# Kernel optimization log

Measured on AMD Instinct MI355X. Metric: run time of the kernel, lower is better.

The kernel has to match this reference:

```python
import jax, jax.numpy as jnp
import numpy as np

B, N, D, H, DG = 1, 1024, 512, 8, 64
DK = D // H
EPS = 1e-5


def _layer_norm(x, g, b):
    m = jnp.mean(x, axis=-1, keepdims=True)
    v = jnp.var(x, axis=-1, keepdims=True)
    return (x - m) / jnp.sqrt(v + EPS) * g + b


def _box_rel_embedding(box):
    # box: (B, N, 4) = x_min, y_min, x_max, y_max
    x_min, y_min, x_max, y_max = [box[..., i] for i in range(4)]  # each (B, N)
    cx = (x_min + x_max) * 0.5
    cy = (y_min + y_max) * 0.5
    w = x_max - x_min + 1.0
    h = y_max - y_min + 1.0
    dx = jnp.log(jnp.clip(jnp.abs((cx[:, :, None] - cx[:, None, :]) / w[:, :, None]), 0.001))
    dy = jnp.log(jnp.clip(jnp.abs((cy[:, :, None] - cy[:, None, :]) / h[:, :, None]), 0.001))
    dw = jnp.log(w[:, :, None] / w[:, None, :])
    dh = jnp.log(h[:, :, None] / h[:, None, :])
    pos = jnp.stack([dx, dy, dw, dh], axis=-1)  # (B, N, N, 4)
    dim_mat = 1.0 / jnp.power(1000.0, jnp.arange(DG // 8, dtype=jnp.float32) / (DG // 8))  # (8,)
    mul = (100.0 * pos[..., None] * dim_mat).reshape(pos.shape[0], pos.shape[1], pos.shape[2], -1)  # (B,N,N,32)
    return jnp.concatenate([jnp.sin(mul), jnp.cos(mul)], axis=-1)  # (B, N, N, 64)


def _split_heads(x, W, b):
    # torch permute(2,0,1,3).view(-1, len, d_k): head-major flattening
    return (x @ W.T + b).reshape(B, N, H, DK).transpose(2, 0, 1, 3).reshape(H * B, N, DK)


def _forward(input_query, input_key, input_value, input_box,
             Wq, bq, Wk, bk, Wv, bv, Wo, bo, WG_w, WG_b,
             ln0_g, ln0_b, ln_g, ln_b):
    residual = input_query
    emb = _box_rel_embedding(input_box)  # (B, N, N, 64)
    # per-head linear (64 -> 1) then relu: (B, H, N, N)
    w_g = jax.nn.relu(jnp.einsum('bijg,hg->bhij', emb, WG_w) + WG_b[None, :, None, None])
    q = _split_heads(input_query, Wq, bq)  # (H*B, N, DK)
    k = _split_heads(input_key, Wk, bk)
    v = _split_heads(input_value, Wv, bv)
    scores = jnp.einsum('xnd,xmd->xnm', q, k) / np.sqrt(DK).astype(np.float32)  # (H*B, N, N)
    # original adds (B,H,N,N) to (H*B,N,N): only valid for B==1
    w_mn = jax.nn.softmax(jnp.log(jnp.clip(w_g.reshape(H * B, N, N), 1e-6)) + scores, axis=-1)
    x = jnp.einsum('xnm,xmd->xnd', w_mn, v)  # (H*B, N, DK)
    # faithful to original: transpose(1,2) then view(nbatches, -1, h*d_k)
    x = x.transpose(0, 2, 1).reshape(B, -1, H * DK)  # (B, N, D)
    out0 = _layer_norm(x + residual, ln0_g, ln0_b)
    out = out0 @ Wo.T + bo  # dropout = identity (eval mode)
    return _layer_norm(out + out0, ln_g, ln_b)


def setup_inputs() -> dict:
    key = jax.random.key(0)
    ks = jax.random.split(key, 12)
    inp = {}
    inp['input_query'] = jax.random.normal(ks[0], (B, N, D), dtype=jnp.float32)
    inp['input_key'] = jax.random.normal(ks[1], (B, N, D), dtype=jnp.float32)
    inp['input_value'] = jax.random.normal(ks[2], (B, N, D), dtype=jnp.float32)
    mins = jax.random.uniform(ks[3], (B, N, 2), dtype=jnp.float32) * 500.0
    sizes = jax.random.uniform(ks[4], (B, N, 2), dtype=jnp.float32) * 99.0 + 1.0
    inp['input_box'] = jnp.concatenate([mins, mins + sizes], axis=-1)  # valid boxes
    s = 0.02
    inp['Wq'] = jax.random.normal(ks[5], (D, D), dtype=jnp.float32) * s
    inp['bq'] = jnp.zeros((D,), dtype=jnp.float32)
    inp['Wk'] = jax.random.normal(ks[6], (D, D), dtype=jnp.float32) * s
    inp['bk'] = jnp.zeros((D,), dtype=jnp.float32)
    inp['Wv'] = jax.random.normal(ks[7], (D, D), dtype=jnp.float32) * s
    inp['bv'] = jnp.zeros((D,), dtype=jnp.float32)
    inp['Wo'] = jax.random.normal(ks[8], (D, D), dtype=jnp.float32) * s
    inp['bo'] = jnp.zeros((D,), dtype=jnp.float32)
    inp['WG_w'] = jax.random.normal(ks[9], (H, DG), dtype=jnp.float32) * 0.1
    inp['WG_b'] = jax.random.normal(ks[10], (H,), dtype=jnp.float32) * 0.1
    inp['ln0_g'] = jnp.ones((D,), dtype=jnp.float32)
    inp['ln0_b'] = jnp.zeros((D,), dtype=jnp.float32)
    inp['ln_g'] = jnp.ones((D,), dtype=jnp.float32)
    inp['ln_b'] = jnp.zeros((D,), dtype=jnp.float32)
    return inp


def reference(input_query, input_key, input_value, input_box,
              Wq, bq, Wk, bk, Wv, bv, Wo, bo, WG_w, WG_b,
              ln0_g, ln0_b, ln_g, ln_b):
    return _forward(input_query, input_key, input_value, input_box,
                    Wq, bq, Wk, bk, Wv, bv, Wo, bo, WG_w, WG_b,
                    ln0_g, ln0_b, ln_g, ln_b)
```

## Files before the change

### kernel.cpp

```cpp
#include <hip/hip_runtime.h>
#include <cstddef>

#define NTOK 1024
#define DMODEL 512
#define NHEAD 8
#define DKH 64
#define NSPLIT 4
#define JQ 256

typedef __attribute__((ext_vector_type(4))) float f32x4;
typedef __attribute__((ext_vector_type(8))) __bf16 bf16x8;
typedef __attribute__((ext_vector_type(4))) __bf16 bf16x4;
typedef __attribute__((ext_vector_type(4))) unsigned short u16x4;
typedef __attribute__((ext_vector_type(8))) unsigned short u16x8;
typedef __attribute__((ext_vector_type(4))) _Float16 f16x4;
typedef unsigned short ushort_t;

__device__ __forceinline__ float wave_sum_f(float v){
  #pragma unroll
  for (int m=1; m<64; m<<=1) v += __shfl_xor(v, m, 64);
  return v;
}
__device__ __forceinline__ unsigned short f2bf(float f){
  __bf16 b = (__bf16)f;
  return __builtin_bit_cast(unsigned short, b);
}
__device__ __forceinline__ float bf2f(unsigned short u){
  return (float)__builtin_bit_cast(__bf16, u);
}

__device__ __forceinline__ float fract_hw(float x){
  float r; asm("v_fract_f32 %0, %1" : "=v"(r) : "v"(x)); return r;
}
__device__ __forceinline__ float sin_rev(float rev){
  float f = fract_hw(rev);
  float s; asm("v_sin_f32 %0, %1" : "=v"(s) : "v"(f)); return s;
}
__device__ __forceinline__ float cos_rev(float rev){
  float f = fract_hw(rev);
  float c; asm("v_cos_f32 %0, %1" : "=v"(c) : "v"(f)); return c;
}
__device__ __forceinline__ float log_hw(float x){
  float l; asm("v_log_f32 %0, %1" : "=v"(l) : "v"(x));
  return 0.69314718056f * l;
}
__device__ __forceinline__ float exp_hw(float x){
  float y = x * 1.44269504f;
  float e; asm("v_exp_f32 %0, %1" : "=v"(e) : "v"(y));
  return e;
}

__global__ __launch_bounds__(256) void k_front2(
    const float* __restrict__ box, const float* __restrict__ WGw, const float* __restrict__ WGb,
    _Float16* __restrict__ wg16,
    const float* __restrict__ inq, const float* __restrict__ ink, const float* __restrict__ inv,
    const float* __restrict__ Wq, const float* __restrict__ Wk, const float* __restrict__ Wv,
    const float* __restrict__ Wo,
    const float* __restrict__ bq, const float* __restrict__ bk, const float* __restrict__ bv,
    ushort_t* __restrict__ Qb, ushort_t* __restrict__ Kb, ushort_t* __restrict__ Vt,
    ushort_t* __restrict__ Wob){
  __shared__ __align__(16) char smem[17408];
  const int t = threadIdx.x;
  const int lane = t & 63, w = t >> 6, li = lane & 15, g = lane >> 4;
  if (blockIdx.x >= 1408){
    int off = ((blockIdx.x - 1408)*256 + t)*8;
    float4 a = *(const float4*)(Wo + off);
    float4 b4 = *(const float4*)(Wo + off + 4);
    u16x4 o0, o1;
    o0[0]=f2bf(a.x); o0[1]=f2bf(a.y); o0[2]=f2bf(a.z); o0[3]=f2bf(a.w);
    o1[0]=f2bf(b4.x); o1[1]=f2bf(b4.y); o1[2]=f2bf(b4.z); o1[3]=f2bf(b4.w);
    *(u16x4*)(Wob + off) = o0;
    *(u16x4*)(Wob + off + 4) = o1;
    return;
  }
  if (blockIdx.x >= 1024){
    const int u = blockIdx.x - 1024;
    const int z = u >> 7;
    const int rem = u & 127;
    const int m0 = (rem >> 3)*64;
    const int n0 = (rem & 7)*64;
    const float* A = z==0 ? inq : z==1 ? ink : inv;
    const float* W = z==0 ? Wq : z==1 ? Wk : Wv;
    const float* bias = z==0 ? bq : z==1 ? bk : bv;
    ushort_t* Al = (ushort_t*)smem;
    ushort_t* Wl = (ushort_t*)(smem + 8704);
    const int row = t >> 2, kq = (t & 3)*16;
    const int mrb = (w >> 1)*32;
    const int nrb = (w & 1)*32;
    f32x4 acc[2][2] = {};
    for (int k0 = 0; k0 < DMODEL; k0 += 64){
      {
        const float* ap = A + (size_t)(m0+row)*DMODEL + k0 + kq;
        const float* wp = W + (size_t)(n0+row)*DMODEL + k0 + kq;
        #pragma unroll
        for (int q=0; q<4; q++){
          float4 av = *(const float4*)(ap + q*4);
          float4 wv = *(const float4*)(wp + q*4);
          u16x4 pa, pw;
          pa[0]=f2bf(av.x); pa[1]=f2bf(av.y); pa[2]=f2bf(av.z); pa[3]=f2bf(av.w);
          pw[0]=f2bf(wv.x); pw[1]=f2bf(wv.y); pw[2]=f2bf(wv.z); pw[3]=f2bf(wv.w);
          *(u16x4*)(Al + row*68 + kq + q*4) = pa;
          *(u16x4*)(Wl + row*68 + kq + q*4) = pw;
        }
      }
      __syncthreads();
      #pragma unroll
      for (int kc=0; kc<64; kc+=32){
        const ushort_t* arl = Al + (mrb + li)*68 + kc + g*8;
        const ushort_t* wrl = Wl + (nrb + li)*68 + kc + g*8;
        bf16x8 af0 = *(const bf16x8*)(arl);
        bf16x8 af1 = *(const bf16x8*)(arl + 16*68);
        bf16x8 wf0 = *(const bf16x8*)(wrl);
        bf16x8 wf1 = *(const bf16x8*)(wrl + 16*68);
        if (z < 2){
          acc[0][0] = __builtin_amdgcn_mfma_f32_16x16x32_bf16(wf0, af0, acc[0][0], 0,0,0);
          acc[0][1] = __builtin_amdgcn_mfma_f32_16x16x32_bf16(wf0, af1, acc[0][1], 0,0,0);
          acc[1][0] = __builtin_amdgcn_mfma_f32_16x16x32_bf16(wf1, af0, acc[1][0], 0,0,0);
          acc[1][1] = __builtin_amdgcn_mfma_f32_16x16x32_bf16(wf1, af1, acc[1][1], 0,0,0);
        } else {
          acc[0][0] = __builtin_amdgcn_mfma_f32_16x16x32_bf16(af0, wf0, acc[0][0], 0,0,0);
          acc[0][1] = __builtin_amdgcn_mfma_f32_16x16x32_bf16(af0, wf1, acc[0][1], 0,0,0);
          acc[1][0] = __builtin_amdgcn_mfma_f32_16x16x32_bf16(af1, wf0, acc[1][0], 0,0,0);
          acc[1][1] = __builtin_amdgcn_mfma_f32_16x16x32_bf16(af1, wf1, acc[1][1], 0,0,0);
        }
      }
      __syncthreads();
    }
    if (z < 2){
      ushort_t* C = z ? Kb : Qb;
      #pragma unroll
      for (int nf=0; nf<2; nf++){
        int n = n0 + nrb + nf*16 + g*4;
        float4 b4 = *(const float4*)(bias + n);
        const float* bp = (const float*)&b4;
        #pragma unroll
        for (int mf=0; mf<2; mf++){
          int m = m0 + mrb + mf*16 + li;
          u16x4 o;
          #pragma unroll
          for (int r=0; r<4; r++) o[r] = f2bf(acc[nf][mf][r] + bp[r]);
          *(u16x4*)(C + (size_t)m*DMODEL + n) = o;
        }
      }
    } else {
      #pragma unroll
      for (int mf=0; mf<2; mf++){
        int m = m0 + mrb + mf*16 + g*4;
        #pragma unroll
        for (int nf=0; nf<2; nf++){
          int n = n0 + nrb + nf*16 + li;
          float bn = bias[n];
          u16x4 o;
          #pragma unroll
          for (int r=0; r<4; r++) o[r] = f2bf(acc[mf][nf][r] + bn);
          *(u16x4*)(Vt + (((size_t)(n>>6))<<16) + ((size_t)(n&63)<<10) + m) = o;
        }
      }
    }
    return;
  }
  float* arr = (float*)smem;
  #pragma unroll
  for (int u2=0; u2<4; u2++){
    int idx = u2*256 + t;
    float4 b4 = *(const float4*)(box + idx*4);
    arr[idx]        = (b4.x + b4.z)*0.5f;
    arr[1024+idx]   = (b4.y + b4.w)*0.5f;
    arr[2048+idx]   = log_hw(b4.z - b4.x + 1.0f);
    arr[3072+idx]   = log_hw(b4.w - b4.y + 1.0f);
  }
  const int i = blockIdx.x;
  float4 bi = *(const float4*)(box + i*4);
  float wi = bi.z - bi.x + 1.0f, hi = bi.w - bi.y + 1.0f;
  float Pi = (g==0) ? (bi.x+bi.z)*0.5f : (g==1) ? (bi.y+bi.w)*0.5f
           : (g==2) ? log_hw(wi) : log_hw(hi);
  float Ri = (g==0) ? 1.0f/wi : (g==1) ? 1.0f/hi : 1.0f;
  const bool doLog = (g < 2);
  bf16x8 wfs = {}, wfc = {};
  float wgb_li = 0.0f;
  if (li < 8){
    #pragma unroll
    for (int e=0; e<8; e++){
      wfs[e] = (__bf16)WGw[li*64 + g*8 + e];
      wfc[e] = (__bf16)WGw[li*64 + 32 + g*8 + e];
    }
    wgb_li = WGb[li];
  }
  __syncthreads();
  const float* parr = arr + g*1024;
  const float DMrev[8] = {15.9154943f, 6.7115094f, 2.8302196f, 1.1934938f,
                          0.5032921f, 0.2122365f, 0.08949941f, 0.0377416f};
  const int jbeg = w*256;
  for (int it=0; it<16; ++it){
    int j = jbeg + it*16 + li;
    float diff = (Pi - parr[j])*Ri;
    float lg = log_hw(fmaxf(fabsf(diff), 1e-3f));
    float dv = doLog ? lg : diff;
    bf16x8 afs, afc;
    #pragma unroll
    for (int e=0; e<8; e++){
      float rev = dv * DMrev[e];
      afs[e] = (__bf16)sin_rev(rev);
      afc[e] = (__bf16)cos_rev(rev);
    }
    f32x4 acc = (f32x4){0.f,0.f,0.f,0.f};
    acc = __builtin_amdgcn_mfma_f32_16x16x32_bf16(afs, wfs, acc, 0,0,0);
    acc = __builtin_amdgcn_mfma_f32_16x16x32_bf16(afc, wfc, acc, 0,0,0);
    if (li < 8){
      f16x4 o;
      #pragma unroll
      for (int r=0; r<4; r++)
        o[r] = (_Float16)fmaxf(acc[r] + wgb_li, 6.103515625e-05f);
      *(f16x4*)(wg16 + (((size_t)li<<20) + ((size_t)i<<10) + jbeg + it*16 + g*4)) = o;
    }
  }
}

__global__ __launch_bounds__(512) void k_attn3(const ushort_t* __restrict__ Qb,
     const ushort_t* __restrict__ Kb, const ushort_t* __restrict__ Vt,
     const _Float16* __restrict__ wg, ushort_t* __restrict__ Xpt, float* __restrict__ rsp){
  __shared__ ushort_t Ks[256*68];
  __shared__ ushort_t Vs[64*264];
  const int t = threadIdx.x;
  const int itg = blockIdx.x, h = blockIdx.y, sp = blockIdx.z;
  const int jbeg = sp*JQ;
  {
    const int r = t >> 3, c = (t & 7)*8;
    #pragma unroll
    for (int p=0; p<4; p++){
      u16x8 kv = *(const u16x8*)(Kb + (size_t)(jbeg + p*64 + r)*DMODEL + h*DKH + c);
      *(u16x8*)(Ks + (p*64 + r)*68 + c) = kv;
      u16x8 vv = *(const u16x8*)(Vt + ((size_t)h<<16) + (size_t)r*NTOK + jbeg + p*64 + c);
      *(u16x8*)(Vs + r*264 + p*64 + c) = vv;
    }
  }
  const int lane = t & 63, w = t >> 6;
  const int i0 = (itg*8 + w)*16;
  const int li = lane & 15, g = lane >> 4;
  const ushort_t* qp = Qb + (size_t)(i0+li)*DMODEL + h*DKH + g*8;
  bf16x8 qf0 = *(const bf16x8*)(qp);
  bf16x8 qf1 = *(const bf16x8*)(qp + 32);
  const _Float16* gbase = wg + ((size_t)h<<20) + ((size_t)(i0+li)<<10) + jbeg + g*4;
  f32x4 xacc[4];
  #pragma unroll
  for (int mf=0; mf<4; mf++) xacc[mf] = (f32x4){0.f,0.f,0.f,0.f};
  float rsum = 0.f;
  __syncthreads();
  #pragma unroll
  for (int jj = 0; jj < JQ; jj += 32){
    const ushort_t* kp = Ks + (jj + li)*68 + g*8;
    bf16x8 a00 = *(const bf16x8*)(kp);
    bf16x8 a01 = *(const bf16x8*)(kp + 32);
    bf16x8 a10 = *(const bf16x8*)(kp + 16*68);
    bf16x8 a11 = *(const bf16x8*)(kp + 16*68 + 32);
    f32x4 s0 = (f32x4){0.f,0.f,0.f,0.f};
    f32x4 s1 = (f32x4){0.f,0.f,0.f,0.f};
    s0 = __builtin_amdgcn_mfma_f32_16x16x32_bf16(a00, qf0, s0, 0,0,0);
    s0 = __builtin_amdgcn_mfma_f32_16x16x32_bf16(a01, qf1, s0, 0,0,0);
    s1 = __builtin_amdgcn_mfma_f32_16x16x32_bf16(a10, qf0, s1, 0,0,0);
    s1 = __builtin_amdgcn_mfma_f32_16x16x32_bf16(a11, qf1, s1, 0,0,0);
    f16x4 g0 = *(const f16x4*)(gbase + jj);
    f16x4 g1 = *(const f16x4*)(gbase + jj + 16);
    float p[8];
    #pragma unroll
    for (int r=0; r<4; r++){ p[r]   = (float)g0[r] * exp_hw(s0[r]*0.125f); rsum += p[r]; }
    #pragma unroll
    for (int r=0; r<4; r++){ p[4+r] = (float)g1[r] * exp_hw(s1[r]*0.125f); rsum += p[4+r]; }
    bf16x8 pb;
    pb[0]=(__bf16)p[0]; pb[1]=(__bf16)p[1]; pb[2]=(__bf16)p[2]; pb[3]=(__bf16)p[3];
    pb[4]=(__bf16)p[4]; pb[5]=(__bf16)p[5]; pb[6]=(__bf16)p[6]; pb[7]=(__bf16)p[7];
    #pragma unroll
    for (int mf=0; mf<4; mf++){
      const ushort_t* vp = Vs + (size_t)(li + mf*16)*264 + jj + g*4;
      bf16x4 lo = *(const bf16x4*)(vp);
      bf16x4 hi = *(const bf16x4*)(vp + 16);
      bf16x8 vf = __builtin_shufflevector(lo, hi, 0,1,2,3,4,5,6,7);
      xacc[mf] = __builtin_amdgcn_mfma_f32_16x16x32_bf16(vf, pb, xacc[mf], 0,0,0);
    }
  }
  rsum += __shfl_xor(rsum, 16, 64);
  rsum += __shfl_xor(rsum, 32, 64);
  if (lane < 16) rsp[((size_t)sp*NHEAD + h)*NTOK + i0 + li] = rsum;
  __syncthreads();
  float* xw = (float*)Ks + w*(16*68);
  #pragma unroll
  for (int mf=0; mf<4; mf++)
    *(f32x4*)&xw[li*68 + mf*16 + g*4] = xacc[mf];
  __builtin_amdgcn_s_waitcnt(0);
  float xv[16];
  #pragma unroll
  for (int r=0; r<16; r++) xv[r] = xw[r*68 + lane];
  u16x8 o0, o1;
  #pragma unroll
  for (int r=0; r<8; r++){ o0[r] = f2bf(xv[r]); o1[r] = f2bf(xv[8+r]); }
  ushort_t* xp = Xpt + (((size_t)sp*NHEAD + h)*DKH + lane)*NTOK + i0;
  *(u16x8*)(xp)     = o0;
  *(u16x8*)(xp + 8) = o1;
}

__global__ __launch_bounds__(512) void k_back2(
    const ushort_t* __restrict__ Xpt, const float* __restrict__ rsp,
    const float* __restrict__ inq,
    const float* __restrict__ ln0g, const float* __restrict__ ln0b,
    const ushort_t* __restrict__ Wob, const float* __restrict__ bo,
    const float* __restrict__ lng, const float* __restrict__ lnb,
    float* __restrict__ out){
  __shared__ ushort_t Ab[8][520];
  __shared__ float    Y[8][516];
  __shared__ float    red[8][8][2];
  const int t = threadIdx.x, lane = t & 63, w = t >> 6;
  const int li = lane & 15, g = lane >> 4;
  const int m0 = blockIdx.x*8;
  {
    const int n = m0 + w;
    const int h = n >> 7, dk = (n >> 1) & 63, mo = (n & 1)*512;
    float x[8];
    float sum = 0.f, sq = 0.f;
    #pragma unroll
    for (int c=0; c<8; c++){
      int d = c*64 + lane;
      int i = mo + d;
      float sv = 0.f, rv = 0.f;
      #pragma unroll
      for (int sp=0; sp<NSPLIT; sp++){
        sv += bf2f(Xpt[(((size_t)sp*NHEAD + h)*DKH + dk)*NTOK + i]);
        rv += rsp[((size_t)sp*NHEAD + h)*NTOK + i];
      }
      x[c] = sv/rv + inq[(size_t)n*DMODEL + d];
      sum += x[c]; sq += x[c]*x[c];
    }
    sum = wave_sum_f(sum);
    sq  = wave_sum_f(sq);
    float mean = sum * (1.0f/512.0f);
    float var = sq * (1.0f/512.0f) - mean*mean;
    float rs = rsqrtf(var + 1e-5f);
    #pragma unroll
    for (int c=0; c<8; c++){
      int d = c*64 + lane;
      float y = (x[c]-mean)*rs*ln0g[d] + ln0b[d];
      Y[w][d] = y;
      Ab[w][d] = f2bf(y);
    }
  }
  __syncthreads();
  const int n0 = w*64;
  const ushort_t* ar = &Ab[li & 7][g*8];
  const ushort_t* wr = Wob + (size_t)(n0+li)*DMODEL + g*8;
  f32x4 acc[4] = {};
  #pragma unroll
  for (int k0=0; k0<DMODEL; k0+=64){
    bf16x8 afa = *(const bf16x8*)(ar + k0);
    bf16x8 afb = *(const bf16x8*)(ar + k0 + 32);
    #pragma unroll
    for (int nf=0; nf<4; nf++){
      const ushort_t* wp = wr + (size_t)nf*16*DMODEL + k0;
      bf16x8 wfa = *(const bf16x8*)(wp);
      bf16x8 wfb = *(const bf16x8*)(wp + 32);
      acc[nf] = __builtin_amdgcn_mfma_f32_16x16x32_bf16(wfa, afa, acc[nf], 0,0,0);
      acc[nf] = __builtin_amdgcn_mfma_f32_16x16x32_bf16(wfb, afb, acc[nf], 0,0,0);
    }
  }
  float s = 0.f, qq = 0.f;
  f32x4 v[4];
  #pragma unroll
  for (int nf=0; nf<4; nf++){
    int n = n0 + nf*16 + g*4;
    f32x4 b4 = *(const f32x4*)(bo + n);
    #pragma unroll
    for (int r=0; r<4; r++){
      float x = acc[nf][r] + b4[r] + Y[li & 7][n + r];
      v[nf][r] = x; s += x; qq += x*x;
    }
  }
  s  += __shfl_xor(s, 16, 64);  s  += __shfl_xor(s, 32, 64);
  qq += __shfl_xor(qq, 16, 64); qq += __shfl_xor(qq, 32, 64);
  if (g == 0 && li < 8){ red[w][li][0] = s; red[w][li][1] = qq; }
  __syncthreads();
  float S = 0.f, Q = 0.f;
  #pragma unroll
  for (int u=0; u<8; u++){ S += red[u][li & 7][0]; Q += red[u][li & 7][1]; }
  float mean = S * (1.0f/512.0f);
  float var = Q * (1.0f/512.0f) - mean*mean;
  float rs = rsqrtf(var + 1e-5f);
  if (li < 8){
    const int m = m0 + li;
    #pragma unroll
    for (int nf=0; nf<4; nf++){
      int n = n0 + nf*16 + g*4;
      f32x4 g4 = *(const f32x4*)(lng + n);
      f32x4 be = *(const f32x4*)(lnb + n);
      f32x4 o;
      #pragma unroll
      for (int r=0; r<4; r++) o[r] = (v[nf][r]-mean)*rs*g4[r] + be[r];
      *(f32x4*)(out + (size_t)m*DMODEL + n) = o;
    }
  }
}

extern "C" void kernel_launch(void* const* d_in, const int* in_sizes, int n_in,
                              void* d_out, int out_size, void* d_ws, size_t ws_size,
                              hipStream_t stream){
  (void)in_sizes; (void)n_in; (void)out_size; (void)ws_size;
  const float* in_q = (const float*)d_in[0];
  const float* in_k = (const float*)d_in[1];
  const float* in_v = (const float*)d_in[2];
  const float* box  = (const float*)d_in[3];
  const float* Wq   = (const float*)d_in[4];
  const float* bq   = (const float*)d_in[5];
  const float* Wk   = (const float*)d_in[6];
  const float* bk   = (const float*)d_in[7];
  const float* Wv   = (const float*)d_in[8];
  const float* bv   = (const float*)d_in[9];
  const float* Wo   = (const float*)d_in[10];
  const float* bo   = (const float*)d_in[11];
  const float* WGw  = (const float*)d_in[12];
  const float* WGb  = (const float*)d_in[13];
  const float* ln0g = (const float*)d_in[14];
  const float* ln0b = (const float*)d_in[15];
  const float* lng  = (const float*)d_in[16];
  const float* lnb  = (const float*)d_in[17];

  float* ws = (float*)d_ws;
  ushort_t* Wob  = (ushort_t*)(ws + 0);
  ushort_t* Qb   = (ushort_t*)(ws + 131072);
  ushort_t* Kb   = (ushort_t*)(ws + 393216);
  ushort_t* Vt   = (ushort_t*)(ws + 655360);
  _Float16* wg16 = (_Float16*)(ws + 917504);
  ushort_t* Xpt  = (ushort_t*)(ws + 5111808);
  float*    rsp  = ws + 6160384;
  float*    out  = (float*)d_out;

  k_front2<<<dim3(1536), dim3(256), 0, stream>>>(box, WGw, WGb, wg16,
            in_q, in_k, in_v, Wq, Wk, Wv, Wo, bq, bk, bv, Qb, Kb, Vt, Wob);
  k_attn3<<<dim3(8,8,4), dim3(512), 0, stream>>>(Qb, Kb, Vt, wg16, Xpt, rsp);
  k_back2<<<dim3(128), dim3(512), 0, stream>>>(Xpt, rsp, in_q, ln0g, ln0b,
            Wob, bo, lng, lnb, out);
}
```

Before: 66.73 us.

## Merge three kernels into one persistent launch with atomic counter barriers

Folds the front, attention and back kernels into a single 1664-block launch at 512 threads. Blocks signal completion through global atomic counters, and the attention and back-end blocks spin on those counters before they start. Front blocks are reshaped to 512 threads, with each QKV GEMM block doing two tiles. This aims to remove inter-kernel launch gaps and tail drain, but it adds a memset launch, spin-wait overhead, a large shared-memory footprint that limits occupancy, and a deadlock risk if waiting blocks are resident before their producers.

```diff
diff --git a/kernel.cpp b/kernel.cpp
--- a/kernel.cpp
+++ b/kernel.cpp
@@ -50,7 +50,20 @@
   return e;
 }
 
-__global__ __launch_bounds__(256) void k_front2(
+__device__ __forceinline__ void mark_done(unsigned* c){
+  __syncthreads();
+  if (threadIdx.x == 0)
+    __hip_atomic_fetch_add(c, 1u, __ATOMIC_RELEASE, __HIP_MEMORY_SCOPE_AGENT);
+}
+__device__ __forceinline__ void wait_for(unsigned* c, unsigned target){
+  if (threadIdx.x == 0){
+    while (__hip_atomic_load(c, __ATOMIC_ACQUIRE, __HIP_MEMORY_SCOPE_AGENT) < target)
+      __builtin_amdgcn_s_sleep(8);
+  }
+  __syncthreads();
+}
+
+__global__ __launch_bounds__(512) void k_all(
     const float* __restrict__ box, const float* __restrict__ WGw, const float* __restrict__ WGb,
     _Float16* __restrict__ wg16,
     const float* __restrict__ inq, const float* __restrict__ ink, const float* __restrict__ inv,
@@ -58,35 +71,91 @@
     const float* __restrict__ Wo,
     const float* __restrict__ bq, const float* __restrict__ bk, const float* __restrict__ bv,
     ushort_t* __restrict__ Qb, ushort_t* __restrict__ Kb, ushort_t* __restrict__ Vt,
-    ushort_t* __restrict__ Wob){
-  __shared__ __align__(16) char smem[17408];
+    ushort_t* __restrict__ Wob,
+    ushort_t* __restrict__ Xpt, float* __restrict__ rsp,
+    const float* __restrict__ ln0g, const float* __restrict__ ln0b,
+    const float* __restrict__ bo, const float* __restrict__ lng, const float* __restrict__ lnb,
+    float* __restrict__ out, unsigned* bar){
+  __shared__ __align__(16) char smem[68608];
   const int t = threadIdx.x;
+  const int b = blockIdx.x;
   const int lane = t & 63, w = t >> 6, li = lane & 15, g = lane >> 4;
-  if (blockIdx.x >= 1408){
-    int off = ((blockIdx.x - 1408)*256 + t)*8;
-    float4 a = *(const float4*)(Wo + off);
-    float4 b4 = *(const float4*)(Wo + off + 4);
-    u16x4 o0, o1;
-    o0[0]=f2bf(a.x); o0[1]=f2bf(a.y); o0[2]=f2bf(a.z); o0[3]=f2bf(a.w);
-    o1[0]=f2bf(b4.x); o1[1]=f2bf(b4.y); o1[2]=f2bf(b4.z); o1[3]=f2bf(b4.w);
-    *(u16x4*)(Wob + off) = o0;
-    *(u16x4*)(Wob + off + 4) = o1;
+
+  if (b < 1024){
+    float* arr = (float*)smem;
+    #pragma unroll
+    for (int u2=0; u2<2; u2++){
+      int idx = u2*512 + t;
+      float4 b4 = *(const float4*)(box + idx*4);
+      arr[idx]        = (b4.x + b4.z)*0.5f;
+      arr[1024+idx]   = (b4.y + b4.w)*0.5f;
+      arr[2048+idx]   = log_hw(b4.z - b4.x + 1.0f);
+      arr[3072+idx]   = log_hw(b4.w - b4.y + 1.0f);
+    }
+    const int i = b;
+    float4 bi = *(const float4*)(box + i*4);
+    float wi = bi.z - bi.x + 1.0f, hi = bi.w - bi.y + 1.0f;
+    float Pi = (g==0) ? (bi.x+bi.z)*0.5f : (g==1) ? (bi.y+bi.w)*0.5f
+             : (g==2) ? log_hw(wi) : log_hw(hi);
+    float Ri = (g==0) ? 1.0f/wi : (g==1) ? 1.0f/hi : 1.0f;
+    const bool doLog = (g < 2);
+    bf16x8 wfs = {}, wfc = {};
+    float wgb_li = 0.0f;
+    if (li < 8){
+      #pragma unroll
+      for (int e=0; e<8; e++){
+        wfs[e] = (__bf16)WGw[li*64 + g*8 + e];
+        wfc[e] = (__bf16)WGw[li*64 + 32 + g*8 + e];
+      }
+      wgb_li = WGb[li];
+    }
+    __syncthreads();
+    const float* parr = arr + g*1024;
+    const float DMrev[8] = {15.9154943f, 6.7115094f, 2.8302196f, 1.1934938f,
+                            0.5032921f, 0.2122365f, 0.08949941f, 0.0377416f};
+    const int jbeg = w*128;
+    for (int it=0; it<8; ++it){
+      int j = jbeg + it*16 + li;
+      float diff = (Pi - parr[j])*Ri;
+      float lg = log_hw(fmaxf(fabsf(diff), 1e-3f));
+      float dv = doLog ? lg : diff;
+      bf16x8 afs, afc;
+      #pragma unroll
+      for (int e=0; e<8; e++){
+        float rev = dv * DMrev[e];
+        afs[e] = (__bf16)sin_rev(rev);
+        afc[e] = (__bf16)cos_rev(rev);
+      }
+      f32x4 acc = (f32x4){0.f,0.f,0.f,0.f};
+      acc = __builtin_amdgcn_mfma_f32_16x16x32_bf16(afs, wfs, acc, 0,0,0);
+      acc = __builtin_amdgcn_mfma_f32_16x16x32_bf16(afc, wfc, acc, 0,0,0);
+      if (li < 8){
+        f16x4 o;
+        #pragma unroll
+        for (int r=0; r<4; r++)
+          o[r] = (_Float16)fmaxf(acc[r] + wgb_li, 6.103515625e-05f);
+        *(f16x4*)(wg16 + (((size_t)li<<20) + ((size_t)i<<10) + jbeg + it*16 + g*4)) = o;
+      }
+    }
+    mark_done(bar);
     return;
   }
-  if (blockIdx.x >= 1024){
-    const int u = blockIdx.x - 1024;
-    const int z = u >> 7;
-    const int rem = u & 127;
+  if (b < 1216){
+    const int unit = (b - 1024)*2 + (w >> 2);
+    const int z = unit >> 7;
+    const int rem = unit & 127;
     const int m0 = (rem >> 3)*64;
     const int n0 = (rem & 7)*64;
     const float* A = z==0 ? inq : z==1 ? ink : inv;
     const float* W = z==0 ? Wq : z==1 ? Wk : Wv;
     const float* bias = z==0 ? bq : z==1 ? bk : bv;
-    ushort_t* Al = (ushort_t*)smem;
-    ushort_t* Wl = (ushort_t*)(smem + 8704);
-    const int row = t >> 2, kq = (t & 3)*16;
-    const int mrb = (w >> 1)*32;
-    const int nrb = (w & 1)*32;
+    ushort_t* Al = (ushort_t*)(smem + (w>>2)*17408);
+    ushort_t* Wl = (ushort_t*)(smem + (w>>2)*17408 + 8704);
+    const int t2 = t & 255;
+    const int row = t2 >> 2, kq = (t2 & 3)*16;
+    const int w2 = w & 3;
+    const int mrb = (w2 >> 1)*32;
+    const int nrb = (w2 & 1)*32;
     f32x4 acc[2][2] = {};
     for (int k0 = 0; k0 < DMODEL; k0 += 64){
       {
@@ -157,242 +226,190 @@
         }
       }
     }
+    mark_done(bar);
     return;
   }
-  float* arr = (float*)smem;
-  #pragma unroll
-  for (int u2=0; u2<4; u2++){
-    int idx = u2*256 + t;
-    float4 b4 = *(const float4*)(box + idx*4);
-    arr[idx]        = (b4.x + b4.z)*0.5f;
-    arr[1024+idx]   = (b4.y + b4.w)*0.5f;
-    arr[2048+idx]   = log_hw(b4.z - b4.x + 1.0f);
-    arr[3072+idx]   = log_hw(b4.w - b4.y + 1.0f);
-  }
-  const int i = blockIdx.x;
-  float4 bi = *(const float4*)(box + i*4);
-  float wi = bi.z - bi.x + 1.0f, hi = bi.w - bi.y + 1.0f;
-  float Pi = (g==0) ? (bi.x+bi.z)*0.5f : (g==1) ? (bi.y+bi.w)*0.5f
-           : (g==2) ? log_hw(wi) : log_hw(hi);
-  float Ri = (g==0) ? 1.0f/wi : (g==1) ? 1.0f/hi : 1.0f;
-  const bool doLog = (g < 2);
-  bf16x8 wfs = {}, wfc = {};
-  float wgb_li = 0.0f;
-  if (li < 8){
-    #pragma unroll
-    for (int e=0; e<8; e++){
-      wfs[e] = (__bf16)WGw[li*64 + g*8 + e];
-      wfc[e] = (__bf16)WGw[li*64 + 32 + g*8 + e];
-    }
-    wgb_li = WGb[li];
-  }
-  __syncthreads();
-  const float* parr = arr + g*1024;
-  const float DMrev[8] = {15.9154943f, 6.7115094f, 2.8302196f, 1.1934938f,
-                          0.5032921f, 0.2122365f, 0.08949941f, 0.0377416f};
-  const int jbeg = w*256;
-  for (int it=0; it<16; ++it){
-    int j = jbeg + it*16 + li;
-    float diff = (Pi - parr[j])*Ri;
-    float lg = log_hw(fmaxf(fabsf(diff), 1e-3f));
-    float dv = doLog ? lg : diff;
-    bf16x8 afs, afc;
-    #pragma unroll
-    for (int e=0; e<8; e++){
-      float rev = dv * DMrev[e];
-      afs[e] = (__bf16)sin_rev(rev);
-      afc[e] = (__bf16)cos_rev(rev);
-    }
-    f32x4 acc = (f32x4){0.f,0.f,0.f,0.f};
-    acc = __builtin_amdgcn_mfma_f32_16x16x32_bf16(afs, wfs, acc, 0,0,0);
-    acc = __builtin_amdgcn_mfma_f32_16x16x32_bf16(afc, wfc, acc, 0,0,0);
-    if (li < 8){
-      f16x4 o;
-      #pragma unroll
-      for (int r=0; r<4; r++)
-        o[r] = (_Float16)fmaxf(acc[r] + wgb_li, 6.103515625e-05f);
-      *(f16x4*)(wg16 + (((size_t)li<<20) + ((size_t)i<<10) + jbeg + it*16 + g*4)) = o;
-    }
-  }
-}
-
-__global__ __launch_bounds__(512) void k_attn3(const ushort_t* __restrict__ Qb,
-     const ushort_t* __restrict__ Kb, const ushort_t* __restrict__ Vt,
-     const _Float16* __restrict__ wg, ushort_t* __restrict__ Xpt, float* __restrict__ rsp){
-  __shared__ ushort_t Ks[256*68];
-  __shared__ ushort_t Vs[64*264];
-  const int t = threadIdx.x;
-  const int itg = blockIdx.x, h = blockIdx.y, sp = blockIdx.z;
-  const int jbeg = sp*JQ;
+  if (b < 1280){
+    int off = ((b - 1216)*512 + t)*8;
+    float4 a = *(const float4*)(Wo + off);
+    float4 b4 = *(const float4*)(Wo + off + 4);
+    u16x4 o0, o1;
+    o0[0]=f2bf(a.x); o0[1]=f2bf(a.y); o0[2]=f2bf(a.z); o0[3]=f2bf(a.w);
+    o1[0]=f2bf(b4.x); o1[1]=f2bf(b4.y); o1[2]=f2bf(b4.z); o1[3]=f2bf(b4.w);
+    *(u16x4*)(Wob + off) = o0;
+    *(u16x4*)(Wob + off + 4) = o1;
+    mark_done(bar);
+    return;
+  }
+  if (b < 1536){
+    wait_for(bar, 1280u);
+    ushort_t* Ks = (ushort_t*)smem;
+    ushort_t* Vs = (ushort_t*)(smem + 34816);
+    const int bb = b - 1280;
+    const int itg = bb & 7, h = (bb >> 3) & 7, sp = bb >> 6;
+    const int jbeg = sp*JQ;
+    {
+      const int r = t >> 3, c = (t & 7)*8;
+      #pragma unroll
+      for (int p=0; p<4; p++){
+        u16x8 kv = *(const u16x8*)(Kb + (size_t)(jbeg + p*64 + r)*DMODEL + h*DKH + c);
+        *(u16x8*)(Ks + (p*64 + r)*68 + c) = kv;
+        u16x8 vv = *(const u16x8*)(Vt + ((size_t)h<<16) + (size_t)r*NTOK + jbeg + p*64 + c);
+        *(u16x8*)(Vs + r*264 + p*64 + c) = vv;
+      }
+    }
+    const int i0 = (itg*8 + w)*16;
+    const ushort_t* qp = Qb + (size_t)(i0+li)*DMODEL + h*DKH + g*8;
+    bf16x8 qf0 = *(const bf16x8*)(qp);
+    bf16x8 qf1 = *(const bf16x8*)(qp + 32);
+    const _Float16* gbase = wg16 + ((size_t)h<<20) + ((size_t)(i0+li)<<10) + jbeg + g*4;
+    f32x4 xacc[4];
+    #pragma unroll
+    for (int mf=0; mf<4; mf++) xacc[mf] = (f32x4){0.f,0.f,0.f,0.f};
+    float rsum = 0.f;
+    __syncthreads();
+    #pragma unroll
+    for (int jj = 0; jj < JQ; jj += 32){
+      const ushort_t* kp = Ks + (jj + li)*68 + g*8;
+      bf16x8 a00 = *(const bf16x8*)(kp);
+      bf16x8 a01 = *(const bf16x8*)(kp + 32);
+      bf16x8 a10 = *(const bf16x8*)(kp + 16*68);
+      bf16x8 a11 = *(const bf16x8*)(kp + 16*68 + 32);
+      f32x4 s0 = (f32x4){0.f,0.f,0.f,0.f};
+      f32x4 s1 = (f32x4){0.f,0.f,0.f,0.f};
+      s0 = __builtin_amdgcn_mfma_f32_16x16x32_bf16(a00, qf0, s0, 0,0,0);
+      s0 = __builtin_amdgcn_mfma_f32_16x16x32_bf16(a01, qf1, s0, 0,0,0);
+      s1 = __builtin_amdgcn_mfma_f32_16x16x32_bf16(a10, qf0, s1, 0,0,0);
+      s1 = __builtin_amdgcn_mfma_f32_16x16x32_bf16(a11, qf1, s1, 0,0,0);
+      f16x4 g0 = *(const f16x4*)(gbase + jj);
+      f16x4 g1 = *(const f16x4*)(gbase + jj + 16);
+      float p[8];
+      #pragma unroll
+      for (int r=0; r<4; r++){ p[r]   = (float)g0[r] * exp_hw(s0[r]*0.125f); rsum += p[r]; }
+      #pragma unroll
+      for (int r=0; r<4; r++){ p[4+r] = (float)g1[r] * exp_hw(s1[r]*0.125f); rsum += p[4+r]; }
+      bf16x8 pb;
+      pb[0]=(__bf16)p[0]; pb[1]=(__bf16)p[1]; pb[2]=(__bf16)p[2]; pb[3]=(__bf16)p[3];
+      pb[4]=(__bf16)p[4]; pb[5]=(__bf16)p[5]; pb[6]=(__bf16)p[6]; pb[7]=(__bf16)p[7];
+      #pragma unroll
+      for (int mf=0; mf<4; mf++){
+        const ushort_t* vp = Vs + (size_t)(li + mf*16)*264 + jj + g*4;
+        bf16x4 lo = *(const bf16x4*)(vp);
+        bf16x4 hi = *(const bf16x4*)(vp + 16);
+        bf16x8 vf = __builtin_shufflevector(lo, hi, 0,1,2,3,4,5,6,7);
+        xacc[mf] = __builtin_amdgcn_mfma_f32_16x16x32_bf16(vf, pb, xacc[mf], 0,0,0);
+      }
+    }
+    rsum += __shfl_xor(rsum, 16, 64);
+    rsum += __shfl_xor(rsum, 32, 64);
+    if (lane < 16) rsp[((size_t)sp*NHEAD + h)*NTOK + i0 + li] = rsum;
+    __syncthreads();
+    float* xw = (float*)Ks + w*(16*68);
+    #pragma unroll
+    for (int mf=0; mf<4; mf++)
+      *(f32x4*)&xw[li*68 + mf*16 + g*4] = xacc[mf];
+    __builtin_amdgcn_s_waitcnt(0);
+    float xv[16];
+    #pragma unroll
+    for (int r=0; r<16; r++) xv[r] = xw[r*68 + lane];
+    u16x8 o0, o1;
+    #pragma unroll
+    for (int r=0; r<8; r++){ o0[r] = f2bf(xv[r]); o1[r] = f2bf(xv[8+r]); }
+    ushort_t* xp = Xpt + (((size_t)sp*NHEAD + h)*DKH + lane)*NTOK + i0;
+    *(u16x8*)(xp)     = o0;
+    *(u16x8*)(xp + 8) = o1;
+    mark_done(bar + 1);
+    return;
+  }
   {
-    const int r = t >> 3, c = (t & 7)*8;
-    #pragma unroll
-    for (int p=0; p<4; p++){
-      u16x8 kv = *(const u16x8*)(Kb + (size_t)(jbeg + p*64 + r)*DMODEL + h*DKH + c);
-      *(u16x8*)(Ks + (p*64 + r)*68 + c) = kv;
-      u16x8 vv = *(const u16x8*)(Vt + ((size_t)h<<16) + (size_t)r*NTOK + jbeg + p*64 + c);
-      *(u16x8*)(Vs + r*264 + p*64 + c) = vv;
-    }
-  }
-  const int lane = t & 63, w = t >> 6;
-  const int i0 = (itg*8 + w)*16;
-  const int li = lane & 15, g = lane >> 4;
-  const ushort_t* qp = Qb + (size_t)(i0+li)*DMODEL + h*DKH + g*8;
-  bf16x8 qf0 = *(const bf16x8*)(qp);
-  bf16x8 qf1 = *(const bf16x8*)(qp + 32);
-  const _Float16* gbase = wg + ((size_t)h<<20) + ((size_t)(i0+li)<<10) + jbeg + g*4;
-  f32x4 xacc[4];
-  #pragma unroll
-  for (int mf=0; mf<4; mf++) xacc[mf] = (f32x4){0.f,0.f,0.f,0.f};
-  float rsum = 0.f;
-  __syncthreads();
-  #pragma unroll
-  for (int jj = 0; jj < JQ; jj += 32){
-    const ushort_t* kp = Ks + (jj + li)*68 + g*8;
-    bf16x8 a00 = *(const bf16x8*)(kp);
-    bf16x8 a01 = *(const bf16x8*)(kp + 32);
-    bf16x8 a10 = *(const bf16x8*)(kp + 16*68);
-    bf16x8 a11 = *(const bf16x8*)(kp + 16*68 + 32);
-    f32x4 s0 = (f32x4){0.f,0.f,0.f,0.f};
-    f32x4 s1 = (f32x4){0.f,0.f,0.f,0.f};
-    s0 = __builtin_amdgcn_mfma_f32_16x16x32_bf16(a00, qf0, s0, 0,0,0);
-    s0 = __builtin_amdgcn_mfma_f32_16x16x32_bf16(a01, qf1, s0, 0,0,0);
-    s1 = __builtin_amdgcn_mfma_f32_16x16x32_bf16(a10, qf0, s1, 0,0,0);
-    s1 = __builtin_amdgcn_mfma_f32_16x16x32_bf16(a11, qf1, s1, 0,0,0);
-    f16x4 g0 = *(const f16x4*)(gbase + jj);
-    f16x4 g1 = *(const f16x4*)(gbase + jj + 16);
-    float p[8];
-    #pragma unroll
-    for (int r=0; r<4; r++){ p[r]   = (float)g0[r] * exp_hw(s0[r]*0.125f); rsum += p[r]; }
-    #pragma unroll
-    for (int r=0; r<4; r++){ p[4+r] = (float)g1[r] * exp_hw(s1[r]*0.125f); rsum += p[4+r]; }
-    bf16x8 pb;
-    pb[0]=(__bf16)p[0]; pb[1]=(__bf16)p[1]; pb[2]=(__bf16)p[2]; pb[3]=(__bf16)p[3];
-    pb[4]=(__bf16)p[4]; pb[5]=(__bf16)p[5]; pb[6]=(__bf16)p[6]; pb[7]=(__bf16)p[7];
-    #pragma unroll
-    for (int mf=0; mf<4; mf++){
-      const ushort_t* vp = Vs + (size_t)(li + mf*16)*264 + jj + g*4;
-      bf16x4 lo = *(const bf16x4*)(vp);
-      bf16x4 hi = *(const bf16x4*)(vp + 16);
-      bf16x8 vf = __builtin_shufflevector(lo, hi, 0,1,2,3,4,5,6,7);
-      xacc[mf] = __builtin_amdgcn_mfma_f32_16x16x32_bf16(vf, pb, xacc[mf], 0,0,0);
-    }
-  }
-  rsum += __shfl_xor(rsum, 16, 64);
-  rsum += __shfl_xor(rsum, 32, 64);
-  if (lane < 16) rsp[((size_t)sp*NHEAD + h)*NTOK + i0 + li] = rsum;
-  __syncthreads();
-  float* xw = (float*)Ks + w*(16*68);
-  #pragma unroll
-  for (int mf=0; mf<4; mf++)
-    *(f32x4*)&xw[li*68 + mf*16 + g*4] = xacc[mf];
-  __builtin_amdgcn_s_waitcnt(0);
-  float xv[16];
-  #pragma unroll
-  for (int r=0; r<16; r++) xv[r] = xw[r*68 + lane];
-  u16x8 o0, o1;
-  #pragma unroll
-  for (int r=0; r<8; r++){ o0[r] = f2bf(xv[r]); o1[r] = f2bf(xv[8+r]); }
-  ushort_t* xp = Xpt + (((size_t)sp*NHEAD + h)*DKH + lane)*NTOK + i0;
-  *(u16x8*)(xp)     = o0;
-  *(u16x8*)(xp + 8) = o1;
-}
-
-__global__ __launch_bounds__(512) void k_back2(
-    const ushort_t* __restrict__ Xpt, const float* __restrict__ rsp,
-    const float* __restrict__ inq,
-    const float* __restrict__ ln0g, const float* __restrict__ ln0b,
-    const ushort_t* __restrict__ Wob, const float* __restrict__ bo,
-    const float* __restrict__ lng, const float* __restrict__ lnb,
-    float* __restrict__ out){
-  __shared__ ushort_t Ab[8][520];
-  __shared__ float    Y[8][516];
-  __shared__ float    red[8][8][2];
-  const int t = threadIdx.x, lane = t & 63, w = t >> 6;
-  const int li = lane & 15, g = lane >> 4;
-  const int m0 = blockIdx.x*8;
-  {
-    const int n = m0 + w;
-    const int h = n >> 7, dk = (n >> 1) & 63, mo = (n & 1)*512;
-    float x[8];
-    float sum = 0.f, sq = 0.f;
-    #pragma unroll
-    for (int c=0; c<8; c++){
-      int d = c*64 + lane;
-      int i = mo + d;
-      float sv = 0.f, rv = 0.f;
-      #pragma unroll
-      for (int sp=0; sp<NSPLIT; sp++){
-        sv += bf2f(Xpt[(((size_t)sp*NHEAD + h)*DKH + dk)*NTOK + i]);
-        rv += rsp[((size_t)sp*NHEAD + h)*NTOK + i];
-      }
-      x[c] = sv/rv + inq[(size_t)n*DMODEL + d];
-      sum += x[c]; sq += x[c]*x[c];
-    }
-    sum = wave_sum_f(sum);
-    sq  = wave_sum_f(sq);
-    float mean = sum * (1.0f/512.0f);
-    float var = sq * (1.0f/512.0f) - mean*mean;
-    float rs = rsqrtf(var + 1e-5f);
-    #pragma unroll
-    for (int c=0; c<8; c++){
-      int d = c*64 + lane;
-      float y = (x[c]-mean)*rs*ln0g[d] + ln0b[d];
-      Y[w][d] = y;
-      Ab[w][d] = f2bf(y);
-    }
-  }
-  __syncthreads();
-  const int n0 = w*64;
-  const ushort_t* ar = &Ab[li & 7][g*8];
-  const ushort_t* wr = Wob + (size_t)(n0+li)*DMODEL + g*8;
-  f32x4 acc[4] = {};
-  #pragma unroll
-  for (int k0=0; k0<DMODEL; k0+=64){
-    bf16x8 afa = *(const bf16x8*)(ar + k0);
-    bf16x8 afb = *(const bf16x8*)(ar + k0 + 32);
-    #pragma unroll
-    for (int nf=0; nf<4; nf++){
-      const ushort_t* wp = wr + (size_t)nf*16*DMODEL + k0;
-      bf16x8 wfa = *(const bf16x8*)(wp);
-      bf16x8 wfb = *(const bf16x8*)(wp + 32);
-      acc[nf] = __builtin_amdgcn_mfma_f32_16x16x32_bf16(wfa, afa, acc[nf], 0,0,0);
-      acc[nf] = __builtin_amdgcn_mfma_f32_16x16x32_bf16(wfb, afb, acc[nf], 0,0,0);
-    }
-  }
-  float s = 0.f, qq = 0.f;
-  f32x4 v[4];
-  #pragma unroll
-  for (int nf=0; nf<4; nf++){
-    int n = n0 + nf*16 + g*4;
-    f32x4 b4 = *(const f32x4*)(bo + n);
-    #pragma unroll
-    for (int r=0; r<4; r++){
-      float x = acc[nf][r] + b4[r] + Y[li & 7][n + r];
-      v[nf][r] = x; s += x; qq += x*x;
-    }
-  }
-  s  += __shfl_xor(s, 16, 64);  s  += __shfl_xor(s, 32, 64);
-  qq += __shfl_xor(qq, 16, 64); qq += __shfl_xor(qq, 32, 64);
-  if (g == 0 && li < 8){ red[w][li][0] = s; red[w][li][1] = qq; }
-  __syncthreads();
-  float S = 0.f, Q = 0.f;
-  #pragma unroll
-  for (int u=0; u<8; u++){ S += red[u][li & 7][0]; Q += red[u][li & 7][1]; }
-  float mean = S * (1.0f/512.0f);
-  float var = Q * (1.0f/512.0f) - mean*mean;
-  float rs = rsqrtf(var + 1e-5f);
-  if (li < 8){
-    const int m = m0 + li;
+    wait_for(bar + 1, 256u);
+    ushort_t* Ab = (ushort_t*)smem;
+    float*    Y  = (float*)(smem + 8320);
+    float*    red= (float*)(smem + 24832);
+    const int m0 = (b - 1536)*8;
+    {
+      const int n = m0 + w;
+      const int h = n >> 7, dk = (n >> 1) & 63, mo = (n & 1)*512;
+      float x[8];
+      float sum = 0.f, sq = 0.f;
+      #pragma unroll
+      for (int c=0; c<8; c++){
+        int d = c*64 + lane;
+        int i = mo + d;
+        float sv = 0.f, rv = 0.f;
+        #pragma unroll
+        for (int sp=0; sp<NSPLIT; sp++){
+          sv += bf2f(Xpt[(((size_t)sp*NHEAD + h)*DKH + dk)*NTOK + i]);
+          rv += rsp[((size_t)sp*NHEAD + h)*NTOK + i];
+        }
+        x[c] = sv/rv + inq[(size_t)n*DMODEL + d];
+        sum += x[c]; sq += x[c]*x[c];
+      }
+      sum = wave_sum_f(sum);
+      sq  = wave_sum_f(sq);
+      float mean = sum * (1.0f/512.0f);
+      float var = sq * (1.0f/512.0f) - mean*mean;
+      float rs = rsqrtf(var + 1e-5f);
+      #pragma unroll
+      for (int c=0; c<8; c++){
+        int d = c*64 + lane;
+        float y = (x[c]-mean)*rs*ln0g[d] + ln0b[d];
+        Y[w*516 + d] = y;
+        Ab[w*520 + d] = f2bf(y);
+      }
+    }
+    __syncthreads();
+    const int n0 = w*64;
+    const ushort_t* ar = Ab + (li & 7)*520 + g*8;
+    const ushort_t* wr = Wob + (size_t)(n0+li)*DMODEL + g*8;
+    f32x4 acc[4] = {};
+    #pragma unroll
+    for (int k0=0; k0<DMODEL; k0+=64){
+      bf16x8 afa = *(const bf16x8*)(ar + k0);
+      bf16x8 afb = *(const bf16x8*)(ar + k0 + 32);
+      #pragma unroll
+      for (int nf=0; nf<4; nf++){
+        const ushort_t* wp = wr + (size_t)nf*16*DMODEL + k0;
+        bf16x8 wfa = *(const bf16x8*)(wp);
+        bf16x8 wfb = *(const bf16x8*)(wp + 32);
+        acc[nf] = __builtin_amdgcn_mfma_f32_16x16x32_bf16(wfa, afa, acc[nf], 0,0,0);
+        acc[nf] = __builtin_amdgcn_mfma_f32_16x16x32_bf16(wfb, afb, acc[nf], 0,0,0);
+      }
+    }
+    float s = 0.f, qq = 0.f;
+    f32x4 v[4];
     #pragma unroll
     for (int nf=0; nf<4; nf++){
       int n = n0 + nf*16 + g*4;
-      f32x4 g4 = *(const f32x4*)(lng + n);
-      f32x4 be = *(const f32x4*)(lnb + n);
-      f32x4 o;
-      #pragma unroll
-      for (int r=0; r<4; r++) o[r] = (v[nf][r]-mean)*rs*g4[r] + be[r];
-      *(f32x4*)(out + (size_t)m*DMODEL + n) = o;
+      f32x4 b4 = *(const f32x4*)(bo + n);
+      #pragma unroll
+      for (int r=0; r<4; r++){
+        float x = acc[nf][r] + b4[r] + Y[(li & 7)*516 + n + r];
+        v[nf][r] = x; s += x; qq += x*x;
+      }
+    }
+    s  += __shfl_xor(s, 16, 64);  s  += __shfl_xor(s, 32, 64);
+    qq += __shfl_xor(qq, 16, 64); qq += __shfl_xor(qq, 32, 64);
+    if (g == 0 && li < 8){ red[(w*8 + li)*2] = s; red[(w*8 + li)*2 + 1] = qq; }
+    __syncthreads();
+    float S = 0.f, Q = 0.f;
+    #pragma unroll
+    for (int u=0; u<8; u++){ S += red[(u*8 + (li & 7))*2]; Q += red[(u*8 + (li & 7))*2 + 1]; }
+    float mean = S * (1.0f/512.0f);
+    float var = Q * (1.0f/512.0f) - mean*mean;
+    float rs = rsqrtf(var + 1e-5f);
+    if (li < 8){
+      const int m = m0 + li;
+      #pragma unroll
+      for (int nf=0; nf<4; nf++){
+        int n = n0 + nf*16 + g*4;
+        f32x4 g4 = *(const f32x4*)(lng + n);
+        f32x4 be = *(const f32x4*)(lnb + n);
+        f32x4 o;
+        #pragma unroll
+        for (int r=0; r<4; r++) o[r] = (v[nf][r]-mean)*rs*g4[r] + be[r];
+        *(f32x4*)(out + (size_t)m*DMODEL + n) = o;
+      }
     }
   }
 }
@@ -428,11 +445,13 @@
   _Float16* wg16 = (_Float16*)(ws + 917504);
   ushort_t* Xpt  = (ushort_t*)(ws + 5111808);
   float*    rsp  = ws + 6160384;
+  unsigned* bar  = (unsigned*)(ws + 6193152);
   float*    out  = (float*)d_out;
 
-  k_front2<<<dim3(1536), dim3(256), 0, stream>>>(box, WGw, WGb, wg16,
-            in_q, in_k, in_v, Wq, Wk, Wv, Wo, bq, bk, bv, Qb, Kb, Vt, Wob);
-  k_attn3<<<dim3(8,8,4), dim3(512), 0, stream>>>(Qb, Kb, Vt, wg16, Xpt, rsp);
-  k_back2<<<dim3(128), dim3(512), 0, stream>>>(Xpt, rsp, in_q, ln0g, ln0b,
-            Wob, bo, lng, lnb, out);
-}
+  hipMemsetAsync(bar, 0, 8, stream);
+  k_all<<<dim3(1664), dim3(512), 0, stream>>>(
+      box, WGw, WGb, wg16,
+      in_q, in_k, in_v, Wq, Wk, Wv, Wo,
+      bq, bk, bv, Qb, Kb, Vt, Wob,
+      Xpt, rsp, ln0g, ln0b, bo, lng, lnb, out, bar);
+}
```

Result: slower. 257.8 us (+286.4%).
